# Kernel optimization log

Measured on AMD Instinct MI355X. Metric: run time of the kernel, lower is better.

The kernel has to match this reference:

```python
import jax, jax.numpy as jnp
import numpy as np

B, H, S, W, F = 16, 4, 8, 256, 16


def setup_inputs() -> dict:
    key = jax.random.key(0)
    kx, kk = jax.random.split(key)
    x = jax.random.normal(kx, (B, S, W, F), dtype=jnp.float32)
    kernel = jax.random.normal(kk, (H, S, S, W), dtype=jnp.float32)
    return {"x": x, "kernel": kernel}


def reference(x, kernel):
    # kernel: [H, S, S, W]; x: [B, S, W, F]
    Hh, Ss, _, Ww = kernel.shape
    r = jnp.arange(Ww)
    # stacked[h,x,y,j,i] = roll(kernel, shifts=j+1)[i] = kernel[(i-(j+1)) % W]
    idx = (r[None, :] - (r[:, None] + 1)) % Ww          # [W(row=j), W(col=i)]
    stacked = kernel[..., idx]                            # [H,S,S,W,W]
    # torch.tril over last two dims: keep col i <= row j
    tri = (r[None, :] <= r[:, None])                      # [W,W]
    stacked = jnp.where(tri, stacked, jnp.zeros((), dtype=stacked.dtype))
    # masked triangular time-mix contraction
    out = jnp.einsum('hxyji,bxif->bhxyjf', stacked, x)    # [B,H,S,S,W,F]
    base = jnp.arange(1, Ww + 1, dtype=out.dtype).reshape(1, 1, 1, 1, Ww, 1)
    out = out / base
    # transform_x: on diagonal series (x==y) roll time dim by 1, zero first step
    diag_mod = jnp.roll(out, 1, axis=4)
    not_first = (r != 0).reshape(1, 1, 1, 1, Ww, 1)
    diag_mod = diag_mod * not_first.astype(out.dtype)
    eye = jnp.eye(Ss, dtype=bool).reshape(1, 1, Ss, Ss, 1, 1)
    return jnp.where(eye, diag_mod, out)
```

## Files before the change

### kernel.cpp

```cpp
#include <hip/hip_runtime.h>
#include <hip/hip_bf16.h>

typedef short short8 __attribute__((ext_vector_type(8)));
typedef float f32x4 __attribute__((ext_vector_type(4)));

union FragAB { unsigned long long l[2]; int i[4]; short8 v; };

__global__ __launch_bounds__(256, 4)
void k_fused(const float* __restrict__ x,
             const float* __restrict__ kern,
             float* __restrict__ out)
{
    __shared__ __align__(16) ushort Xts[64 * 264];
    __shared__ __align__(8)  ushort wforL[4][336];
    __shared__ float rtab[256];

    const int blk = blockIdx.x;
    const int hy = blk & 31;
    const int sx = (blk >> 5) & 7;
    const int nt = blk >> 8;
    const int h = hy >> 3, sy = hy & 7;
    const int diag = (sx == sy) ? 1 : 0;
    const int t = threadIdx.x;

    {
        const float* krow = kern + ((h * 8 + sx) * 8 + sy) * 256;
        #pragma unroll
        for (int s = 0; s < 4; ++s) {
            #pragma unroll
            for (int pass = 0; pass < 2; ++pass) {
                int q = t + pass * 256;
                if (q < 336) {
                    int src = q - s;
                    float v = (src >= 0 && src < 256) ? krow[src] : 0.0f;
                    __hip_bfloat16 hv = __float2bfloat16(v);
                    wforL[s][q] = reinterpret_cast<ushort&>(hv);
                }
            }
        }
    }
    {
        int denom = t + 1 - diag;
        rtab[t] = (denom > 0) ? (1.0f / (float)denom) : 0.0f;
    }
    {
        const float4* xbase = reinterpret_cast<const float4*>(x);
        #pragma unroll
        for (int it = 0; it < 8; ++it) {
            int id = it * 256 + t;
            int fq = id & 3;
            int k2 = (id >> 2) & 127;
            int bl = id >> 9;
            const float4* rowp = xbase + ((size_t)((nt * 4 + bl) * 8 + sx)) * 1024;
            float4 a = rowp[(2 * k2) * 4 + fq];
            float4 cq = rowp[(2 * k2 + 1) * 4 + fq];
            #pragma unroll
            for (int e = 0; e < 4; ++e) {
                float va = (&a.x)[e], vb = (&cq.x)[e];
                __hip_bfloat16 ha = __float2bfloat16(va);
                __hip_bfloat16 hb = __float2bfloat16(vb);
                uint u = (uint)reinterpret_cast<ushort&>(ha) |
                         ((uint)reinterpret_cast<ushort&>(hb) << 16);
                int row = bl * 16 + fq * 4 + e;
                *reinterpret_cast<uint*>(reinterpret_cast<char*>(Xts) + row * 528 + k2 * 4) = u;
            }
        }
    }
    __syncthreads();

    const int lane = t & 63, wid = t >> 6;
    const int laneM = lane & 15, laneG = lane >> 4;
    const int wj0 = wid * 64;

    const char* XtsB = reinterpret_cast<const char*>(Xts);
    const char* WB = reinterpret_cast<const char*>(wforL);
    const int abyte = laneM * 528 + laneG * 16;

    const int w00 = 255 + diag - wj0 - laneM + 8 * laneG;
    const int s = (laneM - diag + 1) & 3;
    const int bB = s * 674 + 2 * w00;

    #pragma unroll
    for (int n = 0; n < 4; ++n) {
        const int kmaxn = wj0 + 16 * (n + 1);

        f32x4 acc[4];
        #pragma unroll
        for (int m = 0; m < 4; ++m) acc[m] = (f32x4){0.0f, 0.0f, 0.0f, 0.0f};

        for (int kc = 0; kc < kmaxn; kc += 32) {
            FragAB bf;
            {
                const char* p = WB + bB + kc * 2 - 32 * n;
                bf.l[0] = *reinterpret_cast<const unsigned long long*>(p);
                bf.l[1] = *reinterpret_cast<const unsigned long long*>(p + 8);
            }
            FragAB af[4];
            #pragma unroll
            for (int m = 0; m < 4; ++m) {
                const int4 raw = *reinterpret_cast<const int4*>(XtsB + abyte + m * 8448 + kc * 2);
                af[m].i[0] = raw.x; af[m].i[1] = raw.y;
                af[m].i[2] = raw.z; af[m].i[3] = raw.w;
            }
            #pragma unroll
            for (int m = 0; m < 4; ++m)
                acc[m] = __builtin_amdgcn_mfma_f32_16x16x32_bf16(
                    af[m].v, bf.v, acc[m], 0, 0, 0);
        }

        const int j = wj0 + 16 * n + laneM;
        const float rt = rtab[j];
        #pragma unroll
        for (int m = 0; m < 4; ++m) {
            const int b_ = nt * 4 + m;
            float* dst = out + (((size_t)(b_ * 4 + h) * 8 + sx) * 8 + sy) * 4096
                         + (size_t)j * 16 + laneG * 4;
            f32x4 v = acc[m] * rt;
            __builtin_nontemporal_store(v, reinterpret_cast<f32x4*>(dst));
        }
    }
}

extern "C" void kernel_launch(void* const* d_in, const int* in_sizes, int n_in,
                              void* d_out, int out_size, void* d_ws, size_t ws_size,
                              hipStream_t stream) {
    const float* x    = (const float*)d_in[0];
    const float* kern = (const float*)d_in[1];
    float* out = (float*)d_out;

    k_fused<<<1024, 256, 0, stream>>>(x, kern, out);
}
```

Measured before the change: 22.59 us.

## Interleave output tiles across waves and share A fragments across four tile groups

Each wave now owns row tiles wb, wb+64, wb+128 and wb+192 instead of a contiguous 64-row range. That balances the triangular work across waves, where the old layout gave wave 3 far more K iterations than wave 0. All four accumulator groups run inside a single K loop, so each A fragment loaded from LDS feeds up to 16 MFMAs instead of 4. The cost is 64 accumulator registers per lane, per-group guards inside the loop, and stores issued partway through the loop.

```diff
diff --git a/kernel.cpp b/kernel.cpp
--- a/kernel.cpp
+++ b/kernel.cpp
@@ -70,53 +70,60 @@
 
     const int lane = t & 63, wid = t >> 6;
     const int laneM = lane & 15, laneG = lane >> 4;
-    const int wj0 = wid * 64;
+    const int wb = wid * 16;
 
     const char* XtsB = reinterpret_cast<const char*>(Xts);
     const char* WB = reinterpret_cast<const char*>(wforL);
     const int abyte = laneM * 528 + laneG * 16;
 
-    const int w00 = 255 + diag - wj0 - laneM + 8 * laneG;
+    const int w000 = 255 + diag - wb - laneM + 8 * laneG;
     const int s = (laneM - diag + 1) & 3;
-    const int bB = s * 674 + 2 * w00;
+    const int bB0 = s * 674 + 2 * w000;
 
+    f32x4 acc[4][4];
     #pragma unroll
-    for (int n = 0; n < 4; ++n) {
-        const int kmaxn = wj0 + 16 * (n + 1);
+    for (int g = 0; g < 4; ++g)
+        #pragma unroll
+        for (int m = 0; m < 4; ++m)
+            acc[g][m] = (f32x4){0.0f, 0.0f, 0.0f, 0.0f};
 
-        f32x4 acc[4];
-        #pragma unroll
-        for (int m = 0; m < 4; ++m) acc[m] = (f32x4){0.0f, 0.0f, 0.0f, 0.0f};
-
-        for (int kc = 0; kc < kmaxn; kc += 32) {
-            FragAB bf;
-            {
-                const char* p = WB + bB + kc * 2 - 32 * n;
-                bf.l[0] = *reinterpret_cast<const unsigned long long*>(p);
-                bf.l[1] = *reinterpret_cast<const unsigned long long*>(p + 8);
-            }
-            FragAB af[4];
-            #pragma unroll
-            for (int m = 0; m < 4; ++m) {
-                const int4 raw = *reinterpret_cast<const int4*>(XtsB + abyte + m * 8448 + kc * 2);
-                af[m].i[0] = raw.x; af[m].i[1] = raw.y;
-                af[m].i[2] = raw.z; af[m].i[3] = raw.w;
-            }
-            #pragma unroll
-            for (int m = 0; m < 4; ++m)
-                acc[m] = __builtin_amdgcn_mfma_f32_16x16x32_bf16(
-                    af[m].v, bf.v, acc[m], 0, 0, 0);
-        }
-
-        const int j = wj0 + 16 * n + laneM;
-        const float rt = rtab[j];
+    const int kend = wb + 208;
+    for (int kc = 0; kc < kend; kc += 32) {
+        FragAB af[4];
         #pragma unroll
         for (int m = 0; m < 4; ++m) {
-            const int b_ = nt * 4 + m;
-            float* dst = out + (((size_t)(b_ * 4 + h) * 8 + sx) * 8 + sy) * 4096
-                         + (size_t)j * 16 + laneG * 4;
-            f32x4 v = acc[m] * rt;
-            __builtin_nontemporal_store(v, reinterpret_cast<f32x4*>(dst));
+            const int4 raw = *reinterpret_cast<const int4*>(XtsB + abyte + m * 8448 + kc * 2);
+            af[m].i[0] = raw.x; af[m].i[1] = raw.y;
+            af[m].i[2] = raw.z; af[m].i[3] = raw.w;
+        }
+        #pragma unroll
+        for (int g = 0; g < 4; ++g) {
+            const int kmaxg = wb + 64 * g + 16;
+            if (kc < kmaxg) {
+                FragAB bf;
+                {
+                    const char* p = WB + (bB0 - 128 * g) + kc * 2;
+                    bf.l[0] = *reinterpret_cast<const unsigned long long*>(p);
+                    bf.l[1] = *reinterpret_cast<const unsigned long long*>(p + 8);
+                }
+                #pragma unroll
+                for (int m = 0; m < 4; ++m)
+                    acc[g][m] = __builtin_amdgcn_mfma_f32_16x16x32_bf16(
+                        af[m].v, bf.v, acc[g][m], 0, 0, 0);
+                if (kc + 32 >= kmaxg) {
+                    const int j = wb + 64 * g + laneM;
+                    const float rt = rtab[j];
+                    #pragma unroll
+                    for (int m = 0; m < 4; ++m) {
+                        const int b_ = nt * 4 + m;
+                        float* dst = out
+                            + (((size_t)(b_ * 4 + h) * 8 + sx) * 8 + sy) * 4096
+                            + (size_t)j * 16 + laneG * 4;
+                        f32x4 v = acc[g][m] * rt;
+                        __builtin_nontemporal_store(v, reinterpret_cast<f32x4*>(dst));
+                    }
+                }
+            }
         }
     }
 }
```

After: 20.67 us. 8.5% less time.
